# Performance work log

Hardware: AMD Instinct MI355X
Metric: run time of the kernel (lower is better)

Reference implementation:

```python
import jax, jax.numpy as jnp
import numpy as np

SEQ_LEN = 1024
DIM = 384
QK_DIM = 64
BATCH = 16


def setup_inputs() -> dict:
    key = jax.random.key(0)
    k_x, k_qw, k_qb, k_kw = jax.random.split(key, 4)
    bound = DIM ** (-0.5)
    x = jax.random.normal(k_x, (BATCH, SEQ_LEN, DIM), dtype=jnp.float32)
    # ColumnLinear params: weight [seq_len, out_features, in_features]
    q_weight = jax.random.uniform(k_qw, (SEQ_LEN, QK_DIM, DIM), minval=-bound, maxval=bound, dtype=jnp.float32)
    q_bias = jnp.zeros((SEQ_LEN, QK_DIM), dtype=jnp.float32)  # init zeros; keep as param
    k_weight = jax.random.uniform(k_kw, (SEQ_LEN, QK_DIM, DIM), minval=-bound, maxval=bound, dtype=jnp.float32)
    attn_bias = jnp.zeros((SEQ_LEN, SEQ_LEN), dtype=jnp.float32)
    return {"x": x, "q_weight": q_weight, "q_bias": q_bias, "k_weight": k_weight, "attn_bias": attn_bias}


def reference(x, q_weight, q_bias, k_weight, attn_bias):
    scale = DIM ** (-0.5)  # note: scale uses dim, not qk_dim
    # per-column (untied) linear projections
    q = scale * (jnp.einsum('bnc,ndc->bnd', x, q_weight) + q_bias)  # [B,S,qk]
    k = jnp.einsum('bnc,ndc->bnd', x, k_weight)                     # [B,S,qk]
    attn = jnp.einsum('bnd,bmd->bnm', q, k) + attn_bias             # [B,S,S]
    attn = jax.nn.softmax(attn, axis=-1)
    out = jnp.einsum('bnm,bmc->bnc', attn, x)                       # value = input
    return out, attn
```

## Files before the change

### kernel.cpp

```cpp
#include <hip/hip_runtime.h>

#define B_  16
#define S_  1024
#define D_  384
#define QK_ 64

typedef __attribute__((ext_vector_type(8))) short bf16x8;
typedef __attribute__((ext_vector_type(4))) short bf16x4;
typedef __attribute__((ext_vector_type(4))) float f32x4;

__device__ __forceinline__ short f2bf(float f) {
  union { float f; unsigned u; } v; v.f = f;
  unsigned r = v.u + 0x7FFFu + ((v.u >> 16) & 1u);
  return (short)(r >> 16);
}

__device__ __forceinline__ bf16x4 cvt4(const float4 v) {
  bf16x4 r;
  r[0] = f2bf(v.x); r[1] = f2bf(v.y); r[2] = f2bf(v.z); r[3] = f2bf(v.w);
  return r;
}

__global__ __launch_bounds__(256) void k_proj(
    const float* __restrict__ x, const float* __restrict__ qw,
    const float* __restrict__ qb, const float* __restrict__ kw,
    unsigned short* __restrict__ Qb, unsigned short* __restrict__ Kb) {
  __shared__ __attribute__((aligned(16))) short xs[16 * 392];

  const int pos  = blockIdx.x >> 1;
  const int half = blockIdx.x & 1;
  const int tid  = threadIdx.x;
  const int lane = tid & 63;
  const int w    = tid >> 6;
  const int col  = lane & 15;
  const int quad = lane >> 4;

#pragma unroll
  for (int r = 0; r < 6; ++r) {
    int li = tid + 256 * r;
    int brow = li / 96, c4 = li % 96;
    float4 v = *(const float4*)&x[(brow * S_ + pos) * D_ + 4 * c4];
    *(bf16x4*)&xs[brow * 392 + 4 * c4] = cvt4(v);
  }
  __syncthreads();

  const float* wsrc = half ? kw : qw;
  const int j = w * 16 + col;
  const float* wrow = &wsrc[((size_t)pos * QK_ + j) * D_];

  f32x4 acc = {0.f, 0.f, 0.f, 0.f};
#pragma unroll
  for (int ks = 0; ks < 12; ++ks) {
    bf16x8 aF = *(const bf16x8*)&xs[col * 392 + ks * 32 + quad * 8];
    float4 w0 = *(const float4*)&wrow[ks * 32 + quad * 8];
    float4 w1 = *(const float4*)&wrow[ks * 32 + quad * 8 + 4];
    bf16x4 lo = cvt4(w0), hi = cvt4(w1);
    bf16x8 bF;
    bF[0] = lo[0]; bF[1] = lo[1]; bF[2] = lo[2]; bF[3] = lo[3];
    bF[4] = hi[0]; bF[5] = hi[1]; bF[6] = hi[2]; bF[7] = hi[3];
    acc = __builtin_amdgcn_mfma_f32_16x16x32_bf16(aF, bF, acc, 0, 0, 0);
  }

  const float SCALE = 0.051031036307982884f;
#pragma unroll
  for (int r = 0; r < 4; ++r) {
    const int brow = quad * 4 + r;
    float v = acc[r];
    if (half == 0) {
      v = SCALE * (v + qb[pos * QK_ + j]);
      Qb[(brow * S_ + pos) * QK_ + j] = (unsigned short)f2bf(v);
    } else {
      Kb[(brow * S_ + pos) * QK_ + j] = (unsigned short)f2bf(v);
    }
  }
}

__global__ __launch_bounds__(256) void k_xt(
    const float* __restrict__ x, unsigned short* __restrict__ Xt) {
  __shared__ float T[32][33];
  const int gid = blockIdx.x;
  const int b  = gid / (32 * 12);
  const int r  = gid % (32 * 12);
  const int jt = r / 12, ct = r % 12;
  const int j0 = jt * 32, c0 = ct * 32;
  const int tx = threadIdx.x & 31, ty = threadIdx.x >> 5;
#pragma unroll
  for (int k = 0; k < 4; ++k)
    T[ty + 8 * k][tx] = x[(size_t)(b * S_ + j0 + ty + 8 * k) * D_ + c0 + tx];
  __syncthreads();
#pragma unroll
  for (int k = 0; k < 4; ++k) {
    int c = ty + 8 * k;
    Xt[((size_t)b * D_ + c0 + c) * S_ + j0 + tx] = (unsigned short)f2bf(T[tx][c]);
  }
}

__global__ __launch_bounds__(256) void k_logits(
    const unsigned short* __restrict__ Qb, const unsigned short* __restrict__ Kb,
    const float* __restrict__ bias, float* __restrict__ attn) {
  __shared__ __attribute__((aligned(16))) short Qs[64 * 72];
  __shared__ __attribute__((aligned(16))) short Ks[64 * 72];
  const int gid0 = blockIdx.x;
  const int gid  = (gid0 & 7) * 512 + (gid0 >> 3);
  const int b = gid >> 8, it = (gid >> 4) & 15, jt = gid & 15;
  const int i0 = it * 64, j0 = jt * 64;
  const int tid = threadIdx.x, lane = tid & 63, w = tid >> 6;
  const int col = lane & 15, quad = lane >> 4;

#pragma unroll
  for (int r = 0; r < 2; ++r) {
    int li = tid + 256 * r;
    int row = li >> 3, q8 = li & 7;
    *(uint4*)&Qs[row * 72 + q8 * 8] =
        *(const uint4*)&Qb[(b * S_ + i0 + row) * QK_ + q8 * 8];
    *(uint4*)&Ks[row * 72 + q8 * 8] =
        *(const uint4*)&Kb[(b * S_ + j0 + row) * QK_ + q8 * 8];
  }
  __syncthreads();

  f32x4 acc[4] = {{0.f,0.f,0.f,0.f},{0.f,0.f,0.f,0.f},
                  {0.f,0.f,0.f,0.f},{0.f,0.f,0.f,0.f}};
#pragma unroll
  for (int ks = 0; ks < 2; ++ks) {
    bf16x8 aF = *(const bf16x8*)&Qs[(w * 16 + col) * 72 + ks * 32 + quad * 8];
#pragma unroll
    for (int s = 0; s < 4; ++s) {
      bf16x8 bF = *(const bf16x8*)&Ks[(s * 16 + col) * 72 + ks * 32 + quad * 8];
      acc[s] = __builtin_amdgcn_mfma_f32_16x16x32_bf16(aF, bF, acc[s], 0, 0, 0);
    }
  }
#pragma unroll
  for (int s = 0; s < 4; ++s) {
    const int j = j0 + s * 16 + col;
#pragma unroll
    for (int r = 0; r < 4; ++r) {
      const int i = i0 + w * 16 + quad * 4 + r;
      attn[(size_t)(b * S_ + i) * S_ + j] = acc[s][r] + bias[i * S_ + j];
    }
  }
}

__global__ __launch_bounds__(256) void k_softmax(float* __restrict__ attn) {
  const int tid = threadIdx.x, lane = tid & 63, w = tid >> 6;
  float* p = attn + (size_t)blockIdx.x * S_;
  float4 v = *(const float4*)&p[tid * 4];
  float m = fmaxf(fmaxf(v.x, v.y), fmaxf(v.z, v.w));
#pragma unroll
  for (int off = 32; off > 0; off >>= 1) m = fmaxf(m, __shfl_xor(m, off));
  __shared__ float redm[4], reds[4];
  if (lane == 0) redm[w] = m;
  __syncthreads();
  m = fmaxf(fmaxf(redm[0], redm[1]), fmaxf(redm[2], redm[3]));
  float4 e;
  e.x = __expf(v.x - m); e.y = __expf(v.y - m);
  e.z = __expf(v.z - m); e.w = __expf(v.w - m);
  float s = e.x + e.y + e.z + e.w;
#pragma unroll
  for (int off = 32; off > 0; off >>= 1) s += __shfl_xor(s, off);
  if (lane == 0) reds[w] = s;
  __syncthreads();
  s = reds[0] + reds[1] + reds[2] + reds[3];
  const float inv = 1.0f / s;
  e.x *= inv; e.y *= inv; e.z *= inv; e.w *= inv;
  *(float4*)&p[tid * 4] = e;
}

__global__ __launch_bounds__(256) void k_out(
    const float* __restrict__ attn, const unsigned short* __restrict__ Xt,
    float* __restrict__ out) {
  __shared__ __attribute__((aligned(16))) short Ps[64 * 72];
  __shared__ __attribute__((aligned(16))) short Xs[128 * 72];
  const int gid0 = blockIdx.x;
  const int gid  = (gid0 & 7) * 96 + (gid0 >> 3);
  const int b = gid / 48, r48 = gid % 48;
  const int it = r48 / 3, ct = r48 % 3;
  const int i0 = it * 64, c0 = ct * 128;
  const int tid = threadIdx.x, lane = tid & 63, w = tid >> 6;
  const int col = lane & 15, quad = lane >> 4;

  const float* pA = &attn[(size_t)(b * S_ + i0) * S_];
  const unsigned short* xA = &Xt[((size_t)b * D_ + c0) * S_];

  f32x4 acc[8] = {{0.f,0.f,0.f,0.f},{0.f,0.f,0.f,0.f},{0.f,0.f,0.f,0.f},
                  {0.f,0.f,0.f,0.f},{0.f,0.f,0.f,0.f},{0.f,0.f,0.f,0.f},
                  {0.f,0.f,0.f,0.f},{0.f,0.f,0.f,0.f}};

  float4 pv[4];
  uint4  xv[4];

#pragma unroll
  for (int r = 0; r < 4; ++r) {
    int li = tid + 256 * r;
    { int ii = li >> 4, f4 = li & 15;
      pv[r] = *(const float4*)&pA[(size_t)ii * S_ + f4 * 4]; }
    { int cc = li >> 3, p8 = li & 7;
      xv[r] = *(const uint4*)&xA[(size_t)cc * S_ + p8 * 8]; }
  }

  for (int t = 0; t < 16; ++t) {
    __syncthreads();
#pragma unroll
    for (int r = 0; r < 4; ++r) {
      int li = tid + 256 * r;
      int ii = li >> 4, f4 = li & 15;
      *(bf16x4*)&Ps[ii * 72 + f4 * 4] = cvt4(pv[r]);
    }
#pragma unroll
    for (int r = 0; r < 4; ++r) {
      int li = tid + 256 * r;
      int cc = li >> 3, p8 = li & 7;
      *(uint4*)&Xs[cc * 72 + p8 * 8] = xv[r];
    }
    __syncthreads();
    if (t < 15) {
      const int j1 = (t + 1) * 64;
#pragma unroll
      for (int r = 0; r < 4; ++r) {
        int li = tid + 256 * r;
        { int ii = li >> 4, f4 = li & 15;
          pv[r] = *(const float4*)&pA[(size_t)ii * S_ + j1 + f4 * 4]; }
        { int cc = li >> 3, p8 = li & 7;
          xv[r] = *(const uint4*)&xA[(size_t)cc * S_ + j1 + p8 * 8]; }
      }
    }
#pragma unroll
    for (int ks = 0; ks < 2; ++ks) {
      bf16x8 aF = *(const bf16x8*)&Ps[(w * 16 + col) * 72 + ks * 32 + quad * 8];
#pragma unroll
      for (int s = 0; s < 8; ++s) {
        bf16x8 bF = *(const bf16x8*)&Xs[(s * 16 + col) * 72 + ks * 32 + quad * 8];
        acc[s] = __builtin_amdgcn_mfma_f32_16x16x32_bf16(aF, bF, acc[s], 0, 0, 0);
      }
    }
  }

#pragma unroll
  for (int s = 0; s < 8; ++s) {
    const int c = c0 + s * 16 + col;
#pragma unroll
    for (int r = 0; r < 4; ++r) {
      const int i = i0 + w * 16 + quad * 4 + r;
      out[(size_t)(b * S_ + i) * D_ + c] = acc[s][r];
    }
  }
}

extern "C" void kernel_launch(void* const* d_in, const int* in_sizes, int n_in,
                              void* d_out, int out_size, void* d_ws, size_t ws_size,
                              hipStream_t stream) {
  const float* x  = (const float*)d_in[0];
  const float* qw = (const float*)d_in[1];
  const float* qb = (const float*)d_in[2];
  const float* kw = (const float*)d_in[3];
  const float* ab = (const float*)d_in[4];

  float* out  = (float*)d_out;
  float* attn = out + (size_t)B_ * S_ * D_;

  unsigned short* Qb = (unsigned short*)d_ws;
  unsigned short* Kb = Qb + (size_t)B_ * S_ * QK_;
  unsigned short* Xt = Kb + (size_t)B_ * S_ * QK_;

  k_proj   <<<2 * S_,        256, 0, stream>>>(x, qw, qb, kw, Qb, Kb);
  k_xt     <<<B_ * 32 * 12,  256, 0, stream>>>(x, Xt);
  k_logits <<<B_ * 16 * 16,  256, 0, stream>>>(Qb, Kb, ab, attn);
  k_softmax<<<B_ * S_,       256, 0, stream>>>(attn);
  k_out    <<<B_ * 16 * 3,   256, 0, stream>>>(attn, Xt, out);
}
```

Before: 381.4 us.

## Fuse logits and softmax into two-pass online-softmax kernel; prefetch projection weights

Replaces the separate logits and softmax kernels with one kernel. Each 64-thread block handles 16 query rows: a first pass over all keys computes running max and sum (online softmax), and a second pass recomputes the logits and writes normalized probabilities directly. This removes writing the raw logits to global memory and reading them back, at the cost of doing the QK MFMA work twice, reading the bias twice, and running 1024 small single-wave blocks that read K straight from global memory. The projection kernel also issues its x loads and a rolling four-step prefetch of weight rows before the bf16 conversion and barrier, to hide load latency.

```diff
diff --git a/kernel.cpp b/kernel.cpp
--- a/kernel.cpp
+++ b/kernel.cpp
@@ -35,26 +35,43 @@
   const int col  = lane & 15;
   const int quad = lane >> 4;
 
+  float4 xv[6];
 #pragma unroll
   for (int r = 0; r < 6; ++r) {
     int li = tid + 256 * r;
     int brow = li / 96, c4 = li % 96;
-    float4 v = *(const float4*)&x[(brow * S_ + pos) * D_ + 4 * c4];
-    *(bf16x4*)&xs[brow * 392 + 4 * c4] = cvt4(v);
-  }
-  __syncthreads();
+    xv[r] = *(const float4*)&x[(brow * S_ + pos) * D_ + 4 * c4];
+  }
 
   const float* wsrc = half ? kw : qw;
   const int j = w * 16 + col;
   const float* wrow = &wsrc[((size_t)pos * QK_ + j) * D_];
 
+  float4 wv[8];
+#pragma unroll
+  for (int ks = 0; ks < 4; ++ks) {
+    wv[2 * ks]     = *(const float4*)&wrow[ks * 32 + quad * 8];
+    wv[2 * ks + 1] = *(const float4*)&wrow[ks * 32 + quad * 8 + 4];
+  }
+
+#pragma unroll
+  for (int r = 0; r < 6; ++r) {
+    int li = tid + 256 * r;
+    int brow = li / 96, c4 = li % 96;
+    *(bf16x4*)&xs[brow * 392 + 4 * c4] = cvt4(xv[r]);
+  }
+  __syncthreads();
+
   f32x4 acc = {0.f, 0.f, 0.f, 0.f};
 #pragma unroll
   for (int ks = 0; ks < 12; ++ks) {
+    const int sl = ks & 3;
     bf16x8 aF = *(const bf16x8*)&xs[col * 392 + ks * 32 + quad * 8];
-    float4 w0 = *(const float4*)&wrow[ks * 32 + quad * 8];
-    float4 w1 = *(const float4*)&wrow[ks * 32 + quad * 8 + 4];
-    bf16x4 lo = cvt4(w0), hi = cvt4(w1);
+    bf16x4 lo = cvt4(wv[2 * sl]), hi = cvt4(wv[2 * sl + 1]);
+    if (ks < 8) {
+      wv[2 * sl]     = *(const float4*)&wrow[(ks + 4) * 32 + quad * 8];
+      wv[2 * sl + 1] = *(const float4*)&wrow[(ks + 4) * 32 + quad * 8 + 4];
+    }
     bf16x8 bF;
     bF[0] = lo[0]; bF[1] = lo[1]; bF[2] = lo[2]; bF[3] = lo[3];
     bF[4] = hi[0]; bF[5] = hi[1]; bF[6] = hi[2]; bF[7] = hi[3];
@@ -95,74 +112,81 @@
   }
 }
 
-__global__ __launch_bounds__(256) void k_logits(
+__global__ __launch_bounds__(64) void k_attn(
     const unsigned short* __restrict__ Qb, const unsigned short* __restrict__ Kb,
     const float* __restrict__ bias, float* __restrict__ attn) {
-  __shared__ __attribute__((aligned(16))) short Qs[64 * 72];
-  __shared__ __attribute__((aligned(16))) short Ks[64 * 72];
-  const int gid0 = blockIdx.x;
-  const int gid  = (gid0 & 7) * 512 + (gid0 >> 3);
-  const int b = gid >> 8, it = (gid >> 4) & 15, jt = gid & 15;
-  const int i0 = it * 64, j0 = jt * 64;
-  const int tid = threadIdx.x, lane = tid & 63, w = tid >> 6;
-  const int col = lane & 15, quad = lane >> 4;
-
-#pragma unroll
-  for (int r = 0; r < 2; ++r) {
-    int li = tid + 256 * r;
-    int row = li >> 3, q8 = li & 7;
-    *(uint4*)&Qs[row * 72 + q8 * 8] =
-        *(const uint4*)&Qb[(b * S_ + i0 + row) * QK_ + q8 * 8];
-    *(uint4*)&Ks[row * 72 + q8 * 8] =
-        *(const uint4*)&Kb[(b * S_ + j0 + row) * QK_ + q8 * 8];
-  }
-  __syncthreads();
-
-  f32x4 acc[4] = {{0.f,0.f,0.f,0.f},{0.f,0.f,0.f,0.f},
-                  {0.f,0.f,0.f,0.f},{0.f,0.f,0.f,0.f}};
-#pragma unroll
-  for (int ks = 0; ks < 2; ++ks) {
-    bf16x8 aF = *(const bf16x8*)&Qs[(w * 16 + col) * 72 + ks * 32 + quad * 8];
+  const int gid   = blockIdx.x;
+  const int b     = gid >> 6;
+  const int i0    = (gid & 63) * 16;
+  const int lane  = threadIdx.x & 63;
+  const int col   = lane & 15, quad = lane >> 4;
+  const int iq    = i0 + quad * 4;
+
+  const unsigned short* qp = &Qb[(size_t)(b * S_ + i0 + col) * QK_];
+  const bf16x8 qf0 = *(const bf16x8*)&qp[quad * 8];
+  const bf16x8 qf1 = *(const bf16x8*)&qp[32 + quad * 8];
+
+  float m[4] = {-3.0e38f, -3.0e38f, -3.0e38f, -3.0e38f};
+  float l[4] = {0.f, 0.f, 0.f, 0.f};
+
+  for (int jt = 0; jt < 16; ++jt) {
+    const int j0 = jt * 64;
+    const unsigned short* kp = &Kb[(size_t)(b * S_ + j0 + col) * QK_];
+    f32x4 acc[4] = {{0.f,0.f,0.f,0.f},{0.f,0.f,0.f,0.f},
+                    {0.f,0.f,0.f,0.f},{0.f,0.f,0.f,0.f}};
 #pragma unroll
     for (int s = 0; s < 4; ++s) {
-      bf16x8 bF = *(const bf16x8*)&Ks[(s * 16 + col) * 72 + ks * 32 + quad * 8];
-      acc[s] = __builtin_amdgcn_mfma_f32_16x16x32_bf16(aF, bF, acc[s], 0, 0, 0);
-    }
-  }
-#pragma unroll
-  for (int s = 0; s < 4; ++s) {
-    const int j = j0 + s * 16 + col;
-#pragma unroll
-    for (int r = 0; r < 4; ++r) {
-      const int i = i0 + w * 16 + quad * 4 + r;
-      attn[(size_t)(b * S_ + i) * S_ + j] = acc[s][r] + bias[i * S_ + j];
-    }
-  }
-}
-
-__global__ __launch_bounds__(256) void k_softmax(float* __restrict__ attn) {
-  const int tid = threadIdx.x, lane = tid & 63, w = tid >> 6;
-  float* p = attn + (size_t)blockIdx.x * S_;
-  float4 v = *(const float4*)&p[tid * 4];
-  float m = fmaxf(fmaxf(v.x, v.y), fmaxf(v.z, v.w));
-#pragma unroll
-  for (int off = 32; off > 0; off >>= 1) m = fmaxf(m, __shfl_xor(m, off));
-  __shared__ float redm[4], reds[4];
-  if (lane == 0) redm[w] = m;
-  __syncthreads();
-  m = fmaxf(fmaxf(redm[0], redm[1]), fmaxf(redm[2], redm[3]));
-  float4 e;
-  e.x = __expf(v.x - m); e.y = __expf(v.y - m);
-  e.z = __expf(v.z - m); e.w = __expf(v.w - m);
-  float s = e.x + e.y + e.z + e.w;
-#pragma unroll
-  for (int off = 32; off > 0; off >>= 1) s += __shfl_xor(s, off);
-  if (lane == 0) reds[w] = s;
-  __syncthreads();
-  s = reds[0] + reds[1] + reds[2] + reds[3];
-  const float inv = 1.0f / s;
-  e.x *= inv; e.y *= inv; e.z *= inv; e.w *= inv;
-  *(float4*)&p[tid * 4] = e;
+      bf16x8 k0 = *(const bf16x8*)&kp[(s * 16) * QK_ + quad * 8];
+      bf16x8 k1 = *(const bf16x8*)&kp[(s * 16) * QK_ + 32 + quad * 8];
+      acc[s] = __builtin_amdgcn_mfma_f32_16x16x32_bf16(qf0, k0, acc[s], 0, 0, 0);
+      acc[s] = __builtin_amdgcn_mfma_f32_16x16x32_bf16(qf1, k1, acc[s], 0, 0, 0);
+    }
+#pragma unroll
+    for (int r = 0; r < 4; ++r) {
+      float sv0 = acc[0][r] + bias[(size_t)(iq + r) * S_ + j0 + 0 * 16 + col];
+      float sv1 = acc[1][r] + bias[(size_t)(iq + r) * S_ + j0 + 1 * 16 + col];
+      float sv2 = acc[2][r] + bias[(size_t)(iq + r) * S_ + j0 + 2 * 16 + col];
+      float sv3 = acc[3][r] + bias[(size_t)(iq + r) * S_ + j0 + 3 * 16 + col];
+      float t = fmaxf(fmaxf(sv0, sv1), fmaxf(sv2, sv3));
+#pragma unroll
+      for (int off = 8; off >= 1; off >>= 1) t = fmaxf(t, __shfl_xor(t, off));
+      const float mn = fmaxf(m[r], t);
+      float sum = __expf(sv0 - mn) + __expf(sv1 - mn) +
+                  __expf(sv2 - mn) + __expf(sv3 - mn);
+#pragma unroll
+      for (int off = 8; off >= 1; off >>= 1) sum += __shfl_xor(sum, off);
+      l[r] = l[r] * __expf(m[r] - mn) + sum;
+      m[r] = mn;
+    }
+  }
+
+  float inv[4];
+#pragma unroll
+  for (int r = 0; r < 4; ++r) inv[r] = 1.0f / l[r];
+
+  for (int jt = 0; jt < 16; ++jt) {
+    const int j0 = jt * 64;
+    const unsigned short* kp = &Kb[(size_t)(b * S_ + j0 + col) * QK_];
+    f32x4 acc[4] = {{0.f,0.f,0.f,0.f},{0.f,0.f,0.f,0.f},
+                    {0.f,0.f,0.f,0.f},{0.f,0.f,0.f,0.f}};
+#pragma unroll
+    for (int s = 0; s < 4; ++s) {
+      bf16x8 k0 = *(const bf16x8*)&kp[(s * 16) * QK_ + quad * 8];
+      bf16x8 k1 = *(const bf16x8*)&kp[(s * 16) * QK_ + 32 + quad * 8];
+      acc[s] = __builtin_amdgcn_mfma_f32_16x16x32_bf16(qf0, k0, acc[s], 0, 0, 0);
+      acc[s] = __builtin_amdgcn_mfma_f32_16x16x32_bf16(qf1, k1, acc[s], 0, 0, 0);
+    }
+#pragma unroll
+    for (int r = 0; r < 4; ++r) {
+#pragma unroll
+      for (int s = 0; s < 4; ++s) {
+        const float sv = acc[s][r] +
+            bias[(size_t)(iq + r) * S_ + j0 + s * 16 + col];
+        attn[(size_t)(b * S_ + iq + r) * S_ + j0 + s * 16 + col] =
+            __expf(sv - m[r]) * inv[r];
+      }
+    }
+  }
 }
 
 __global__ __launch_bounds__(256) void k_out(
@@ -261,9 +285,8 @@
   unsigned short* Kb = Qb + (size_t)B_ * S_ * QK_;
   unsigned short* Xt = Kb + (size_t)B_ * S_ * QK_;
 
-  k_proj   <<<2 * S_,        256, 0, stream>>>(x, qw, qb, kw, Qb, Kb);
-  k_xt     <<<B_ * 32 * 12,  256, 0, stream>>>(x, Xt);
-  k_logits <<<B_ * 16 * 16,  256, 0, stream>>>(Qb, Kb, ab, attn);
-  k_softmax<<<B_ * S_,       256, 0, stream>>>(attn);
-  k_out    <<<B_ * 16 * 3,   256, 0, stream>>>(attn, Xt, out);
-}
+  k_proj <<<2 * S_,       256, 0, stream>>>(x, qw, qb, kw, Qb, Kb);
+  k_xt   <<<B_ * 32 * 12, 256, 0, stream>>>(x, Xt);
+  k_attn <<<B_ * 64,       64, 0, stream>>>(Qb, Kb, ab, attn);
+  k_out  <<<B_ * 16 * 3,  256, 0, stream>>>(attn, Xt, out);
+}
```

Measured after the change: 381.1 us. About the same (-0.1%).
